# Kernel optimization log

Hardware: AMD Instinct MI355X
Metric: run time of the kernel (lower is better)

## Reference

```python
import jax, jax.numpy as jnp
import numpy as np

HIDDEN = 1024
B, S = 4, 2048


def setup_inputs() -> dict:
    key = jax.random.key(0)
    ks = jax.random.split(key, 8)
    scale = 1.0 / np.sqrt(HIDDEN)
    return {
        "hidden_states": jax.random.normal(ks[0], (B, S, HIDDEN), dtype=jnp.float32),
        "attention_mask": jnp.zeros((B, S, S), dtype=jnp.float32),
        "Wq": jax.random.normal(ks[1], (HIDDEN, HIDDEN), dtype=jnp.float32) * scale,
        "bq": jnp.zeros((HIDDEN,), dtype=jnp.float32),
        "Wk": jax.random.normal(ks[2], (HIDDEN, HIDDEN), dtype=jnp.float32) * scale,
        "bk": jnp.zeros((HIDDEN,), dtype=jnp.float32),
        "Wv": jax.random.normal(ks[3], (HIDDEN, HIDDEN), dtype=jnp.float32) * scale,
        "bv": jnp.zeros((HIDDEN,), dtype=jnp.float32),
    }


def reference(hidden_states, attention_mask, Wq, bq, Wk, bk, Wv, bv):
    # Dense projections (note: no head split in the original module)
    q = jnp.einsum('bsd,de->bse', hidden_states, Wq) + bq  # [B,S,H]
    k = jnp.einsum('bsd,de->bse', hidden_states, Wk) + bk
    v = jnp.einsum('bsd,de->bse', hidden_states, Wv) + bv
    # scores scaled by sqrt(hidden_size) (not per-head dim), per the source
    inv_scale = 1.0 / jnp.sqrt(jnp.asarray(q.shape[-1], dtype=q.dtype))
    scores = jnp.einsum('bqd,bkd->bqk', q, k) * inv_scale  # [B,S,S]
    scores = scores + attention_mask
    weights = jax.nn.softmax(scores, axis=-1)
    # dropout is identity (training=False)
    out = jnp.einsum('bqk,bkd->bqd', weights, v)  # [B,S,H]
    return out
```

## Files before the change

kernel.cpp:

```cpp
#include <hip/hip_runtime.h>
#include <stdint.h>

typedef __attribute__((ext_vector_type(8))) short short8;
typedef __attribute__((ext_vector_type(8))) unsigned short u16x8;
typedef __attribute__((ext_vector_type(4))) float f32x4;

__device__ __forceinline__ uint16_t f2bf(float x) {
  uint32_t u = __float_as_uint(x);
  uint32_t r = (u + 0x7FFFu + ((u >> 16) & 1u)) >> 16;
  return (uint16_t)r;
}
__device__ __forceinline__ float bf2f(uint16_t x) {
  return __uint_as_float(((uint32_t)x) << 16);
}

__device__ __forceinline__ void gl_lds16(const uint16_t* g, void* l) {
  __builtin_amdgcn_global_load_lds(
      (const __attribute__((address_space(1))) void*)g,
      (__attribute__((address_space(3))) void*)l, 16, 0, 0);
}


__global__ __launch_bounds__(256) void cvt_f32_to_bf16(const float* __restrict__ in,
                                                       uint16_t* __restrict__ out) {
  long i = ((long)blockIdx.x * 256 + threadIdx.x) * 8;
  f32x4 v0 = *(const f32x4*)(in + i);
  f32x4 v1 = *(const f32x4*)(in + i + 4);
  u16x8 o;
  o[0] = f2bf(v0[0]); o[1] = f2bf(v0[1]); o[2] = f2bf(v0[2]); o[3] = f2bf(v0[3]);
  o[4] = f2bf(v1[0]); o[5] = f2bf(v1[1]); o[6] = f2bf(v1[2]); o[7] = f2bf(v1[3]);
  *(u16x8*)(out + i) = o;
}

__global__ __launch_bounds__(64) void cvt_w_transpose(const float* __restrict__ W0,
                                                      const float* __restrict__ W1,
                                                      const float* __restrict__ W2,
                                                      uint16_t* __restrict__ WT) {
  const int z = blockIdx.z;
  const float* W = (z == 0) ? W0 : ((z == 1) ? W1 : W2);
  uint16_t* out = WT + (long)z * 1024 * 1024;
  const int n = blockIdx.x * 64 + threadIdx.x;
  const int k0 = blockIdx.y * 128;
  for (int kk = 0; kk < 128; kk += 8) {
    u16x8 o;
#pragma unroll
    for (int j = 0; j < 8; j++) o[j] = f2bf(W[(long)(k0 + kk + j) * 1024 + n]);
    *(u16x8*)(out + (long)n * 1024 + k0 + kk) = o;
  }
}

__global__ __launch_bounds__(256) void transpose_v(const uint16_t* __restrict__ V,
                                                   uint16_t* __restrict__ Vt) {
  __shared__ uint16_t tile[64][66];
  const int b = blockIdx.z;
  const int s0 = blockIdx.x * 64, d0 = blockIdx.y * 64;
  const int t = threadIdx.x;
  const int r = t >> 3, c = (t & 7) * 8;
  const uint16_t* Vb = V + (long)b * 2048 * 1024;
#pragma unroll
  for (int j = 0; j < 2; j++) {
    u16x8 v = *(const u16x8*)(Vb + (long)(s0 + r + 32 * j) * 1024 + d0 + c);
#pragma unroll
    for (int i = 0; i < 8; i++) tile[r + 32 * j][c + i] = v[i];
  }
  __syncthreads();
  uint16_t* Vtb = Vt + (long)b * 1024 * 2048;
#pragma unroll
  for (int j = 0; j < 2; j++) {
    const int d = r + 32 * j;
    u16x8 o;
#pragma unroll
    for (int i = 0; i < 8; i++) o[i] = tile[c + i][d];
    *(u16x8*)(Vtb + (long)(d0 + d) * 2048 + s0 + c) = o;
  }
}

__global__ __launch_bounds__(256) void rowsum_inv(const uint16_t* __restrict__ E,
                                                  float* __restrict__ invl) {
  const long row = blockIdx.x;
  const uint16_t* src = E + row * 2048;
  const int t = threadIdx.x;
  u16x8 v = *(const u16x8*)(src + t * 8);
  float s = 0.f;
#pragma unroll
  for (int i = 0; i < 8; i++) s += bf2f(v[i]);
#pragma unroll
  for (int off = 32; off >= 1; off >>= 1) s += __shfl_xor(s, off);
  __shared__ float red[4];
  if ((t & 63) == 0) red[t >> 6] = s;
  __syncthreads();
  if (t == 0) {
    invl[row] = 1.0f / (red[0] + red[1] + red[2] + red[3]);
  }
}

template <int MODE, int AI>
__global__ __launch_bounds__(512, 2) void gemmX(
    const uint16_t* __restrict__ Abase, long sAz,
    const uint16_t* __restrict__ Bbase, long sBz,
    int K, int N,
    char* __restrict__ Cbase, long sCz,
    const float* __restrict__ e0, const float* __restrict__ e1,
    const float* __restrict__ e2,
    const float* __restrict__ maskb, long sMz, float scale,
    const float* __restrict__ rowinv) {
  constexpr int BM = AI * 32;
  constexpr int ABYTES = BM * 128;
  constexpr int BUFB = ABYTES + 32768;
  __shared__ __align__(16) char lds[2 * BUFB];
  const int t = threadIdx.x;
  const int lane = t & 63;
  const int w = t >> 6;
  const int bm = blockIdx.x, bn = blockIdx.y, bz = blockIdx.z;
  const uint16_t* A = (const uint16_t*)((const char*)Abase + (long)bz * sAz);
  const uint16_t* B = (const uint16_t*)((const char*)Bbase + (long)bz * sBz);

  const int srow = t >> 3;
  const int scol = ((((t & 7) * 16) ^ ((srow & 7) << 4)) >> 1);
  const uint16_t* gA[4];
  const uint16_t* gB[4];
#pragma unroll
  for (int s = 0; s < 4; s++) {
    gA[s] = A + (long)(bm * BM + (s % (AI / 2)) * 64 + srow) * K + scol;
    gB[s] = B + (long)(bn * 256 + s * 64 + srow) * K + scol;
  }

  const int wm = w >> 2, wn = w & 3;
  const int fr = lane & 15, kg = lane >> 4;
  const int X = (fr & 7) << 4;
  const int aRow = (wm * (AI * 16) + fr) * 128 + kg * 16;
  const int bRow = (wn * 64 + fr) * 128 + kg * 16;

  f32x4 acc[AI][4];
#pragma unroll
  for (int i = 0; i < AI; i++)
#pragma unroll
    for (int j = 0; j < 4; j++) acc[i][j] = (f32x4){0.f, 0.f, 0.f, 0.f};

  short8 aR[4][2], bR[2][2];
  const int NT = K >> 6;

#define ARD(off, i, ks) (*(const short8*)(lds + (off) + ((aRow + (i) * 2048 + (ks) * 64) ^ X)))
#define BRD(off, j, ks) (*(const short8*)(lds + ABYTES + (off) + ((bRow + (j) * 2048 + (ks) * 64) ^ X)))
#define STG_A01(off, ko) { gl_lds16(gA[0] + (ko), lds + (off) + w * 1024); \
                           gl_lds16(gA[1] + (ko), lds + (off) + 8192 + w * 1024); }
#define STG_A23(off, ko) { gl_lds16(gA[2] + (ko), lds + (off) + 16384 + w * 1024); \
                           gl_lds16(gA[3] + (ko), lds + (off) + 24576 + w * 1024); }
#define STG_B01(off, ko) { gl_lds16(gB[0] + (ko), lds + ABYTES + (off) + w * 1024); \
                           gl_lds16(gB[1] + (ko), lds + ABYTES + (off) + 8192 + w * 1024); }
#define STG_B23(off, ko) { gl_lds16(gB[2] + (ko), lds + ABYTES + (off) + 16384 + w * 1024); \
                           gl_lds16(gB[3] + (ko), lds + ABYTES + (off) + 24576 + w * 1024); }
#define LGKM0 { asm volatile("s_waitcnt lgkmcnt(0)" ::: "memory"); __builtin_amdgcn_sched_barrier(0); }
#define MFMA16(I0, J0)                                                            \
  __builtin_amdgcn_s_setprio(1);                                                  \
  _Pragma("unroll") for (int i = 0; i < 4; i++)                                   \
  _Pragma("unroll") for (int j = 0; j < 2; j++)                                   \
  _Pragma("unroll") for (int ks = 0; ks < 2; ks++)                                \
    acc[(I0) + i][(J0) + j] = __builtin_amdgcn_mfma_f32_16x16x32_bf16(            \
        aR[i][ks], bR[j][ks], acc[(I0) + i][(J0) + j], 0, 0, 0);                  \
  __builtin_amdgcn_s_setprio(0);

  if constexpr (AI == 8) { STG_A01(0, 0); STG_A23(0, 0); }
  else                   { STG_A01(0, 0); }
  STG_B01(0, 0); STG_B23(0, 0);

  int curo = 0;
  for (int tt = 0; tt < NT - 1; ++tt) {
    const int nxto = curo ^ BUFB;
    const int ko = (tt + 1) << 6;
    if constexpr (AI == 8) {
      STG_A01(nxto, ko);
      asm volatile("s_waitcnt vmcnt(2)" ::: "memory");
      __builtin_amdgcn_s_barrier();
      __builtin_amdgcn_sched_barrier(0);
#pragma unroll
      for (int i = 0; i < 4; i++) { aR[i][0] = ARD(curo, i, 0); aR[i][1] = ARD(curo, i, 1); }
#pragma unroll
      for (int j = 0; j < 2; j++) { bR[j][0] = BRD(curo, j, 0); bR[j][1] = BRD(curo, j, 1); }
      LGKM0;
      MFMA16(0, 0);
      __builtin_amdgcn_s_barrier();
      STG_A23(nxto, ko);
#pragma unroll
      for (int j = 0; j < 2; j++) { bR[j][0] = BRD(curo, 2 + j, 0); bR[j][1] = BRD(curo, 2 + j, 1); }
      __builtin_amdgcn_s_barrier();
      LGKM0;
      MFMA16(0, 2);
      __builtin_amdgcn_s_barrier();
      STG_B01(nxto, ko);
#pragma unroll
      for (int i = 0; i < 4; i++) { aR[i][0] = ARD(curo, 4 + i, 0); aR[i][1] = ARD(curo, 4 + i, 1); }
      __builtin_amdgcn_s_barrier();
      LGKM0;
      MFMA16(4, 2);
      __builtin_amdgcn_s_barrier();
      STG_B23(nxto, ko);
#pragma unroll
      for (int j = 0; j < 2; j++) { bR[j][0] = BRD(curo, j, 0); bR[j][1] = BRD(curo, j, 1); }
      __builtin_amdgcn_s_barrier();
      LGKM0;
      MFMA16(4, 0);
      __builtin_amdgcn_s_barrier();
    } else {
      STG_A01(nxto, ko);
      STG_B01(nxto, ko);
      asm volatile("s_waitcnt vmcnt(4)" ::: "memory");
      __builtin_amdgcn_s_barrier();
      __builtin_amdgcn_sched_barrier(0);
#pragma unroll
      for (int i = 0; i < 4; i++) { aR[i][0] = ARD(curo, i, 0); aR[i][1] = ARD(curo, i, 1); }
#pragma unroll
      for (int j = 0; j < 2; j++) { bR[j][0] = BRD(curo, j, 0); bR[j][1] = BRD(curo, j, 1); }
      LGKM0;
      MFMA16(0, 0);
      __builtin_amdgcn_s_barrier();
      STG_B23(nxto, ko);
#pragma unroll
      for (int j = 0; j < 2; j++) { bR[j][0] = BRD(curo, 2 + j, 0); bR[j][1] = BRD(curo, 2 + j, 1); }
      __builtin_amdgcn_s_barrier();
      LGKM0;
      MFMA16(0, 2);
      __builtin_amdgcn_s_barrier();
    }
    curo = nxto;
  }
  asm volatile("s_waitcnt vmcnt(0)" ::: "memory");
  __builtin_amdgcn_s_barrier();
  __builtin_amdgcn_sched_barrier(0);
  if constexpr (AI == 8) {
#pragma unroll
    for (int i = 0; i < 4; i++) { aR[i][0] = ARD(curo, i, 0); aR[i][1] = ARD(curo, i, 1); }
#pragma unroll
    for (int j = 0; j < 2; j++) { bR[j][0] = BRD(curo, j, 0); bR[j][1] = BRD(curo, j, 1); }
    LGKM0;
    MFMA16(0, 0);
#pragma unroll
    for (int j = 0; j < 2; j++) { bR[j][0] = BRD(curo, 2 + j, 0); bR[j][1] = BRD(curo, 2 + j, 1); }
    LGKM0;
    MFMA16(0, 2);
#pragma unroll
    for (int i = 0; i < 4; i++) { aR[i][0] = ARD(curo, 4 + i, 0); aR[i][1] = ARD(curo, 4 + i, 1); }
    LGKM0;
    MFMA16(4, 2);
#pragma unroll
    for (int j = 0; j < 2; j++) { bR[j][0] = BRD(curo, j, 0); bR[j][1] = BRD(curo, j, 1); }
    LGKM0;
    MFMA16(4, 0);
  } else {
#pragma unroll
    for (int i = 0; i < 4; i++) { aR[i][0] = ARD(curo, i, 0); aR[i][1] = ARD(curo, i, 1); }
#pragma unroll
    for (int j = 0; j < 2; j++) { bR[j][0] = BRD(curo, j, 0); bR[j][1] = BRD(curo, j, 1); }
    LGKM0;
    MFMA16(0, 0);
#pragma unroll
    for (int j = 0; j < 2; j++) { bR[j][0] = BRD(curo, 2 + j, 0); bR[j][1] = BRD(curo, 2 + j, 1); }
    LGKM0;
    MFMA16(0, 2);
  }

  const int row0 = bm * BM + wm * (AI * 16) + (kg << 2);
  if (MODE == 0) {
    const int zz = bn >> 2;
    const float* bias = (zz == 0) ? e0 : ((zz == 1) ? e1 : e2);
    uint16_t* C = (uint16_t*)(Cbase + (long)zz * sCz);
    const int cb = (bn & 3) * 256 + wn * 64 + fr;
#pragma unroll
    for (int i = 0; i < AI; i++) {
#pragma unroll
      for (int j = 0; j < 4; j++) {
        const float bv_ = bias[cb + j * 16];
#pragma unroll
        for (int r = 0; r < 4; r++) {
          C[(long)(row0 + i * 16 + r) * 1024 + cb + j * 16] = f2bf(acc[i][j][r] + bv_);
        }
      }
    }
  } else if (MODE == 1) {
    const int col0 = bn * 256 + wn * 64 + fr;
    uint16_t* C = (uint16_t*)(Cbase + (long)bz * sCz);
    const float* mk = (const float*)((const char*)maskb + (long)bz * sMz);
#pragma unroll
    for (int i = 0; i < AI; i++) {
#pragma unroll
      for (int j = 0; j < 4; j++) {
#pragma unroll
        for (int r = 0; r < 4; r++) {
          const long idx = (long)(row0 + i * 16 + r) * N + col0 + j * 16;
          C[idx] = f2bf(__expf(acc[i][j][r] * scale + mk[idx]));
        }
      }
    }
  } else {
    const int col0 = bn * 256 + wn * 64 + fr;
    float* C = (float*)(Cbase + (long)bz * sCz);
    const float* ri = rowinv + (long)bz * 2048;
#pragma unroll
    for (int i = 0; i < AI; i++) {
#pragma unroll
      for (int j = 0; j < 4; j++) {
#pragma unroll
        for (int r = 0; r < 4; r++) {
          const int row = row0 + i * 16 + r;
          C[(long)row * N + col0 + j * 16] = acc[i][j][r] * ri[row];
        }
      }
    }
  }
#undef ARD
#undef BRD
#undef STG_A01
#undef STG_A23
#undef STG_B01
#undef STG_B23
#undef LGKM0
#undef MFMA16
}

extern "C" void kernel_launch(void* const* d_in, const int* in_sizes, int n_in,
                              void* d_out, int out_size, void* d_ws, size_t ws_size,
                              hipStream_t stream) {
  const float* hs = (const float*)d_in[0];
  const float* mask = (const float*)d_in[1];
  const float* Wq = (const float*)d_in[2];
  const float* bq = (const float*)d_in[3];
  const float* Wk = (const float*)d_in[4];
  const float* bk = (const float*)d_in[5];
  const float* Wv = (const float*)d_in[6];
  const float* bv = (const float*)d_in[7];
  float* out = (float*)d_out;

  char* ws = (char*)d_ws;
  uint16_t* hsb = (uint16_t*)ws;
  uint16_t* WT = (uint16_t*)(ws + (16L << 20));
  uint16_t* QKV = (uint16_t*)(ws + (22L << 20));
  uint16_t* Vt = (uint16_t*)(ws + (70L << 20));
  uint16_t* E = (uint16_t*)(ws + (86L << 20));
  float* invl = (float*)(ws + (118L << 20));

  cvt_f32_to_bf16<<<4096, 256, 0, stream>>>(hs, hsb);
  cvt_w_transpose<<<dim3(16, 8, 3), 64, 0, stream>>>(Wq, Wk, Wv, WT);
  gemmX<0, 4><<<dim3(64, 12, 1), 512, 0, stream>>>(
      hsb, 0L, WT, 0L, 1024, 3072, (char*)QKV, 16L << 20,
      bq, bk, bv, nullptr, 0L, 0.f, nullptr);
  transpose_v<<<dim3(32, 16, 4), 256, 0, stream>>>(QKV + 2L * 8192 * 1024, Vt);
  gemmX<1, 8><<<dim3(8, 8, 4), 512, 0, stream>>>(
      QKV, 4L << 20, QKV + 8192L * 1024, 4L << 20, 1024, 2048, (char*)E, 8L << 20,
      nullptr, nullptr, nullptr, mask, 16L << 20, 0.03125f, nullptr);
  rowsum_inv<<<8192, 256, 0, stream>>>(E, invl);
  gemmX<2, 4><<<dim3(16, 4, 4), 512, 0, stream>>>(
      E, 8L << 20, Vt, 4L << 20, 2048, 1024, (char*)out, 8L << 20,
      nullptr, nullptr, nullptr, nullptr, 0L, 0.f, invl);
}
```

Before: 191.5 us.

## Stage GEMM epilogues through LDS, fuse softmax rowsum via atomics, preload B fragments

```diff
diff --git a/kernel.cpp b/kernel.cpp
--- a/kernel.cpp
+++ b/kernel.cpp
@@ -75,25 +75,6 @@
   }
 }
 
-__global__ __launch_bounds__(256) void rowsum_inv(const uint16_t* __restrict__ E,
-                                                  float* __restrict__ invl) {
-  const long row = blockIdx.x;
-  const uint16_t* src = E + row * 2048;
-  const int t = threadIdx.x;
-  u16x8 v = *(const u16x8*)(src + t * 8);
-  float s = 0.f;
-#pragma unroll
-  for (int i = 0; i < 8; i++) s += bf2f(v[i]);
-#pragma unroll
-  for (int off = 32; off >= 1; off >>= 1) s += __shfl_xor(s, off);
-  __shared__ float red[4];
-  if ((t & 63) == 0) red[t >> 6] = s;
-  __syncthreads();
-  if (t == 0) {
-    invl[row] = 1.0f / (red[0] + red[1] + red[2] + red[3]);
-  }
-}
-
 template <int MODE, int AI>
 __global__ __launch_bounds__(512, 2) void gemmX(
     const uint16_t* __restrict__ Abase, long sAz,
@@ -103,7 +84,7 @@
     const float* __restrict__ e0, const float* __restrict__ e1,
     const float* __restrict__ e2,
     const float* __restrict__ maskb, long sMz, float scale,
-    const float* __restrict__ rowinv) {
+    float* __restrict__ lsum) {
   constexpr int BM = AI * 32;
   constexpr int ABYTES = BM * 128;
   constexpr int BUFB = ABYTES + 32768;
@@ -137,7 +118,7 @@
 #pragma unroll
     for (int j = 0; j < 4; j++) acc[i][j] = (f32x4){0.f, 0.f, 0.f, 0.f};
 
-  short8 aR[4][2], bR[2][2];
+  short8 aR[4][2], bR[4][2];
   const int NT = K >> 6;
 
 #define ARD(off, i, ks) (*(const short8*)(lds + (off) + ((aRow + (i) * 2048 + (ks) * 64) ^ X)))
@@ -157,7 +138,7 @@
   _Pragma("unroll") for (int j = 0; j < 2; j++)                                   \
   _Pragma("unroll") for (int ks = 0; ks < 2; ks++)                                \
     acc[(I0) + i][(J0) + j] = __builtin_amdgcn_mfma_f32_16x16x32_bf16(            \
-        aR[i][ks], bR[j][ks], acc[(I0) + i][(J0) + j], 0, 0, 0);                  \
+        aR[i][ks], bR[(J0) + j][ks], acc[(I0) + i][(J0) + j], 0, 0, 0);           \
   __builtin_amdgcn_s_setprio(0);
 
   if constexpr (AI == 8) { STG_A01(0, 0); STG_A23(0, 0); }
@@ -176,15 +157,12 @@
 #pragma unroll
       for (int i = 0; i < 4; i++) { aR[i][0] = ARD(curo, i, 0); aR[i][1] = ARD(curo, i, 1); }
 #pragma unroll
-      for (int j = 0; j < 2; j++) { bR[j][0] = BRD(curo, j, 0); bR[j][1] = BRD(curo, j, 1); }
+      for (int j = 0; j < 4; j++) { bR[j][0] = BRD(curo, j, 0); bR[j][1] = BRD(curo, j, 1); }
       LGKM0;
       MFMA16(0, 0);
       __builtin_amdgcn_s_barrier();
       STG_A23(nxto, ko);
-#pragma unroll
-      for (int j = 0; j < 2; j++) { bR[j][0] = BRD(curo, 2 + j, 0); bR[j][1] = BRD(curo, 2 + j, 1); }
-      __builtin_amdgcn_s_barrier();
-      LGKM0;
+      __builtin_amdgcn_s_barrier();
       MFMA16(0, 2);
       __builtin_amdgcn_s_barrier();
       STG_B01(nxto, ko);
@@ -195,10 +173,7 @@
       MFMA16(4, 2);
       __builtin_amdgcn_s_barrier();
       STG_B23(nxto, ko);
-#pragma unroll
-      for (int j = 0; j < 2; j++) { bR[j][0] = BRD(curo, j, 0); bR[j][1] = BRD(curo, j, 1); }
-      __builtin_amdgcn_s_barrier();
-      LGKM0;
+      __builtin_amdgcn_s_barrier();
       MFMA16(4, 0);
       __builtin_amdgcn_s_barrier();
     } else {
@@ -210,15 +185,12 @@
 #pragma unroll
       for (int i = 0; i < 4; i++) { aR[i][0] = ARD(curo, i, 0); aR[i][1] = ARD(curo, i, 1); }
 #pragma unroll
-      for (int j = 0; j < 2; j++) { bR[j][0] = BRD(curo, j, 0); bR[j][1] = BRD(curo, j, 1); }
+      for (int j = 0; j < 4; j++) { bR[j][0] = BRD(curo, j, 0); bR[j][1] = BRD(curo, j, 1); }
       LGKM0;
       MFMA16(0, 0);
       __builtin_amdgcn_s_barrier();
       STG_B23(nxto, ko);
-#pragma unroll
-      for (int j = 0; j < 2; j++) { bR[j][0] = BRD(curo, 2 + j, 0); bR[j][1] = BRD(curo, 2 + j, 1); }
-      __builtin_amdgcn_s_barrier();
-      LGKM0;
+      __builtin_amdgcn_s_barrier();
       MFMA16(0, 2);
       __builtin_amdgcn_s_barrier();
     }
@@ -227,85 +199,114 @@
   asm volatile("s_waitcnt vmcnt(0)" ::: "memory");
   __builtin_amdgcn_s_barrier();
   __builtin_amdgcn_sched_barrier(0);
+#pragma unroll
+  for (int i = 0; i < 4; i++) { aR[i][0] = ARD(curo, i, 0); aR[i][1] = ARD(curo, i, 1); }
+#pragma unroll
+  for (int j = 0; j < 4; j++) { bR[j][0] = BRD(curo, j, 0); bR[j][1] = BRD(curo, j, 1); }
+  LGKM0;
+  MFMA16(0, 0);
+  MFMA16(0, 2);
   if constexpr (AI == 8) {
-#pragma unroll
-    for (int i = 0; i < 4; i++) { aR[i][0] = ARD(curo, i, 0); aR[i][1] = ARD(curo, i, 1); }
-#pragma unroll
-    for (int j = 0; j < 2; j++) { bR[j][0] = BRD(curo, j, 0); bR[j][1] = BRD(curo, j, 1); }
-    LGKM0;
-    MFMA16(0, 0);
-#pragma unroll
-    for (int j = 0; j < 2; j++) { bR[j][0] = BRD(curo, 2 + j, 0); bR[j][1] = BRD(curo, 2 + j, 1); }
-    LGKM0;
-    MFMA16(0, 2);
 #pragma unroll
     for (int i = 0; i < 4; i++) { aR[i][0] = ARD(curo, 4 + i, 0); aR[i][1] = ARD(curo, 4 + i, 1); }
     LGKM0;
     MFMA16(4, 2);
-#pragma unroll
-    for (int j = 0; j < 2; j++) { bR[j][0] = BRD(curo, j, 0); bR[j][1] = BRD(curo, j, 1); }
-    LGKM0;
     MFMA16(4, 0);
-  } else {
-#pragma unroll
-    for (int i = 0; i < 4; i++) { aR[i][0] = ARD(curo, i, 0); aR[i][1] = ARD(curo, i, 1); }
-#pragma unroll
-    for (int j = 0; j < 2; j++) { bR[j][0] = BRD(curo, j, 0); bR[j][1] = BRD(curo, j, 1); }
-    LGKM0;
-    MFMA16(0, 0);
-#pragma unroll
-    for (int j = 0; j < 2; j++) { bR[j][0] = BRD(curo, 2 + j, 0); bR[j][1] = BRD(curo, 2 + j, 1); }
-    LGKM0;
-    MFMA16(0, 2);
-  }
-
-  const int row0 = bm * BM + wm * (AI * 16) + (kg << 2);
-  if (MODE == 0) {
+  }
+
+  __syncthreads();
+  constexpr int RS = 260;
+  float* eL = (float*)lds;
+  const int wboff = wm * (16 * RS) + (kg * 4) * RS + wn * 64 + fr;
+  const int lr = t >> 4, slab = lr >> 4, row16 = lr & 15, cj = t & 15;
+  const float* rb = eL + slab * (16 * RS) + row16 * RS + cj * 16;
+  const int grow_base = bm * BM + slab * (AI * 16) + row16;
+
+  f32x4 bias4[4];
+  const uint16_t* Cu16 = nullptr;
+  float* Cf32 = nullptr;
+  uint16_t* Cw = nullptr;
+  int colg = 0;
+  const float* mk = nullptr;
+  if constexpr (MODE == 0) {
     const int zz = bn >> 2;
     const float* bias = (zz == 0) ? e0 : ((zz == 1) ? e1 : e2);
-    uint16_t* C = (uint16_t*)(Cbase + (long)zz * sCz);
-    const int cb = (bn & 3) * 256 + wn * 64 + fr;
-#pragma unroll
-    for (int i = 0; i < AI; i++) {
-#pragma unroll
-      for (int j = 0; j < 4; j++) {
-        const float bv_ = bias[cb + j * 16];
-#pragma unroll
-        for (int r = 0; r < 4; r++) {
-          C[(long)(row0 + i * 16 + r) * 1024 + cb + j * 16] = f2bf(acc[i][j][r] + bv_);
-        }
+    colg = (bn & 3) * 256 + cj * 16;
+#pragma unroll
+    for (int q = 0; q < 4; q++) bias4[q] = *(const f32x4*)(bias + colg + q * 4);
+    Cw = (uint16_t*)(Cbase + (long)zz * sCz);
+  } else if constexpr (MODE == 1) {
+    colg = bn * 256 + cj * 16;
+    Cw = (uint16_t*)(Cbase + (long)bz * sCz);
+    mk = (const float*)((const char*)maskb + (long)bz * sMz);
+  } else {
+    colg = bn * 256 + cj * 16;
+    Cf32 = (float*)(Cbase + (long)bz * sCz);
+  }
+  (void)Cu16;
+
+#pragma unroll
+  for (int i = 0; i < AI; i++) {
+#pragma unroll
+    for (int j = 0; j < 4; j++)
+#pragma unroll
+      for (int r = 0; r < 4; r++)
+        eL[wboff + r * RS + j * 16] = acc[i][j][r];
+    __syncthreads();
+    f32x4 v0 = *(const f32x4*)(rb);
+    f32x4 v1 = *(const f32x4*)(rb + 4);
+    f32x4 v2 = *(const f32x4*)(rb + 8);
+    f32x4 v3 = *(const f32x4*)(rb + 12);
+    const int grow = grow_base + i * 16;
+    if constexpr (MODE == 0) {
+      v0 += bias4[0]; v1 += bias4[1]; v2 += bias4[2]; v3 += bias4[3];
+      u16x8 o0, o1;
+#pragma unroll
+      for (int q = 0; q < 4; q++) {
+        o0[q] = f2bf(v0[q]); o0[4 + q] = f2bf(v1[q]);
+        o1[q] = f2bf(v2[q]); o1[4 + q] = f2bf(v3[q]);
       }
+      uint16_t* dst = Cw + (long)grow * 1024 + colg;
+      *(u16x8*)dst = o0;
+      *(u16x8*)(dst + 8) = o1;
+    } else if constexpr (MODE == 1) {
+      const float* mrow = mk + (long)grow * N + colg;
+      f32x4 m0 = *(const f32x4*)(mrow);
+      f32x4 m1 = *(const f32x4*)(mrow + 4);
+      f32x4 m2 = *(const f32x4*)(mrow + 8);
+      f32x4 m3 = *(const f32x4*)(mrow + 12);
+      float e[16];
+#pragma unroll
+      for (int q = 0; q < 4; q++) {
+        e[q] = __expf(v0[q] * scale + m0[q]);
+        e[4 + q] = __expf(v1[q] * scale + m1[q]);
+        e[8 + q] = __expf(v2[q] * scale + m2[q]);
+        e[12 + q] = __expf(v3[q] * scale + m3[q]);
+      }
+      float ps = 0.f;
+#pragma unroll
+      for (int q = 0; q < 16; q++) ps += e[q];
+      ps += __shfl_xor(ps, 1);
+      ps += __shfl_xor(ps, 2);
+      ps += __shfl_xor(ps, 4);
+      ps += __shfl_xor(ps, 8);
+      if ((lane & 15) == 0) atomicAdd(lsum + (long)bz * 2048 + grow, ps);
+      u16x8 o0, o1;
+#pragma unroll
+      for (int q = 0; q < 8; q++) { o0[q] = f2bf(e[q]); o1[q] = f2bf(e[8 + q]); }
+      uint16_t* dst = Cw + (long)grow * N + colg;
+      *(u16x8*)dst = o0;
+      *(u16x8*)(dst + 8) = o1;
+    } else {
+      const float ri = 1.0f / lsum[(long)bz * 2048 + grow];
+      v0 *= ri; v1 *= ri; v2 *= ri; v3 *= ri;
+      float* dst = Cf32 + (long)grow * N + colg;
+      *(f32x4*)dst = v0;
+      *(f32x4*)(dst + 4) = v1;
+      *(f32x4*)(dst + 8) = v2;
+      *(f32x4*)(dst + 12) = v3;
     }
-  } else if (MODE == 1) {
-    const int col0 = bn * 256 + wn * 64 + fr;
-    uint16_t* C = (uint16_t*)(Cbase + (long)bz * sCz);
-    const float* mk = (const float*)((const char*)maskb + (long)bz * sMz);
-#pragma unroll
-    for (int i = 0; i < AI; i++) {
-#pragma unroll
-      for (int j = 0; j < 4; j++) {
-#pragma unroll
-        for (int r = 0; r < 4; r++) {
-          const long idx = (long)(row0 + i * 16 + r) * N + col0 + j * 16;
-          C[idx] = f2bf(__expf(acc[i][j][r] * scale + mk[idx]));
-        }
-      }
-    }
-  } else {
-    const int col0 = bn * 256 + wn * 64 + fr;
-    float* C = (float*)(Cbase + (long)bz * sCz);
-    const float* ri = rowinv + (long)bz * 2048;
-#pragma unroll
-    for (int i = 0; i < AI; i++) {
-#pragma unroll
-      for (int j = 0; j < 4; j++) {
-#pragma unroll
-        for (int r = 0; r < 4; r++) {
-          const int row = row0 + i * 16 + r;
-          C[(long)row * N + col0 + j * 16] = acc[i][j][r] * ri[row];
-        }
-      }
-    }
+    __syncthreads();
   }
 #undef ARD
 #undef BRD
@@ -336,19 +337,19 @@
   uint16_t* QKV = (uint16_t*)(ws + (22L << 20));
   uint16_t* Vt = (uint16_t*)(ws + (70L << 20));
   uint16_t* E = (uint16_t*)(ws + (86L << 20));
-  float* invl = (float*)(ws + (118L << 20));
+  float* lsum = (float*)(ws + (118L << 20));
 
   cvt_f32_to_bf16<<<4096, 256, 0, stream>>>(hs, hsb);
   cvt_w_transpose<<<dim3(16, 8, 3), 64, 0, stream>>>(Wq, Wk, Wv, WT);
+  hipMemsetAsync((void*)lsum, 0, 4L * 2048 * sizeof(float), stream);
   gemmX<0, 4><<<dim3(64, 12, 1), 512, 0, stream>>>(
       hsb, 0L, WT, 0L, 1024, 3072, (char*)QKV, 16L << 20,
       bq, bk, bv, nullptr, 0L, 0.f, nullptr);
   transpose_v<<<dim3(32, 16, 4), 256, 0, stream>>>(QKV + 2L * 8192 * 1024, Vt);
   gemmX<1, 8><<<dim3(8, 8, 4), 512, 0, stream>>>(
       QKV, 4L << 20, QKV + 8192L * 1024, 4L << 20, 1024, 2048, (char*)E, 8L << 20,
-      nullptr, nullptr, nullptr, mask, 16L << 20, 0.03125f, nullptr);
-  rowsum_inv<<<8192, 256, 0, stream>>>(E, invl);
+      nullptr, nullptr, nullptr, mask, 16L << 20, 0.03125f, lsum);
   gemmX<2, 4><<<dim3(16, 4, 4), 512, 0, stream>>>(
       E, 8L << 20, Vt, 4L << 20, 2048, 1024, (char*)out, 8L << 20,
-      nullptr, nullptr, nullptr, nullptr, 0L, 0.f, invl);
-}
+      nullptr, nullptr, nullptr, nullptr, 0L, 0.f, lsum);
+}
```

After: 194.1 us. Within noise of the previous version (+1.3%).
